# Performance work log

Measured on AMD Instinct MI355X. Metric: run time of the kernel, lower is better.

The kernel has to match this reference:

```python
import jax, jax.numpy as jnp
import numpy as np

D = 64  # hidden_dim


def _bn(x, gamma, beta):
    # eval-mode BatchNorm1d with running_mean=0, running_var=1 (fresh model)
    return gamma * x + beta


def _edge_conv(h, W, b, gamma, beta):
    # h: [B,N,D]; W: [2D,D] split into Wi (acts on x_i) and Wj (acts on x_j)
    Wi, Wj = W[:D], W[D:]
    ti = jnp.einsum('bnd,de->bne', h, Wi)  # [B,N,D] (i term)
    tj = jnp.einsum('bmd,de->bme', h, Wj)  # [B,N,D] (j term)
    # e[b,i,j,:] = x_i@Wi + x_j@Wj + b  -> relu -> BN -> max over j
    e = ti[:, :, None, :] + tj[:, None, :, :] + b  # [B,N,N,D]
    e = _bn(jax.nn.relu(e), gamma, beta)
    return e.max(axis=2)  # [B,N,D]


def setup_inputs() -> dict:
    key = jax.random.key(0)
    ks = jax.random.split(key, 16)
    s = lambda k, shp, sc: (jax.random.normal(k, shp, dtype=jnp.float32) * sc)
    inp = {
        'x': s(ks[0], (32, 256, 4), 1.0),
        'W1': s(ks[1], (4, D), 0.5), 'b1': s(ks[2], (D,), 0.1),
        'g1': 1.0 + s(ks[3], (D,), 0.1), 'beta1': s(ks[4], (D,), 0.1),
        'We1': s(ks[5], (2 * D, D), 0.1), 'be1': s(ks[6], (D,), 0.1),
        'ge1': 1.0 + s(ks[7], (D,), 0.1), 'betae1': s(ks[8], (D,), 0.1),
        'We2': s(ks[9], (2 * D, D), 0.1), 'be2': s(ks[10], (D,), 0.1),
        'ge2': 1.0 + s(ks[11], (D,), 0.1), 'betae2': s(ks[12], (D,), 0.1),
        'Wg1': s(ks[13], (2 * D, D), 0.1), 'bg1': s(ks[14], (D,), 0.1),
        'Wg2': s(ks[15], (D, 2), 0.1), 'bg2': jnp.zeros((2,), jnp.float32),
    }
    return inp


def reference(x, W1, b1, g1, beta1, We1, be1, ge1, betae1, We2, be2, ge2, betae2, Wg1, bg1, Wg2, bg2):
    # input MLP: Linear -> ReLU -> BN (eval)
    h = _bn(jax.nn.relu(x @ W1 + b1), g1, beta1)  # [B,N,D]
    h = _edge_conv(h, We1, be1, ge1, betae1)
    h = _edge_conv(h, We2, be2, ge2, betae2)
    x_mean = h.mean(axis=1)  # [B,D]
    x_max = h.max(axis=1)    # [B,D]
    xg = jnp.concatenate([x_mean, x_max], axis=-1)  # [B,2D]
    # global MLP (dropout is identity in eval)
    out = jax.nn.relu(xg @ Wg1 + bg1) @ Wg2 + bg2  # [B,2]
    return out
```

## Files before the change

### kernel.cpp

```cpp
#include <hip/hip_runtime.h>

#define NB 32
#define NN 256
#define DD 64
#define GG 4
#define NPB 64


__global__ __launch_bounds__(512) void k_conv1(
    const float* __restrict__ x,
    const float* __restrict__ W1,  const float* __restrict__ b1,
    const float* __restrict__ g1,  const float* __restrict__ beta1,
    const float* __restrict__ We1,
    float* __restrict__ TI, float* __restrict__ PMAX, float* __restrict__ PMIN)
{
    __shared__ float Hs[NPB * 65];
    const int b  = blockIdx.x >> 2;
    const int g  = blockIdx.x & 3;
    const int l  = threadIdx.x & 63;
    const int w  = __builtin_amdgcn_readfirstlane(threadIdx.x >> 6);
    const int n  = g * NPB + l;
    const int d0 = w * 8;

    {
        float4 xv = *(const float4*)(x + ((size_t)b * NN + n) * 4);
        float a[8];
#pragma unroll
        for (int j = 0; j < 8; ++j) a[j] = b1[d0 + j];
#pragma unroll
        for (int j = 0; j < 8; ++j) a[j] = fmaf(xv.x, W1[0 * DD + d0 + j], a[j]);
#pragma unroll
        for (int j = 0; j < 8; ++j) a[j] = fmaf(xv.y, W1[1 * DD + d0 + j], a[j]);
#pragma unroll
        for (int j = 0; j < 8; ++j) a[j] = fmaf(xv.z, W1[2 * DD + d0 + j], a[j]);
#pragma unroll
        for (int j = 0; j < 8; ++j) a[j] = fmaf(xv.w, W1[3 * DD + d0 + j], a[j]);
#pragma unroll
        for (int j = 0; j < 8; ++j)
            Hs[l * 65 + d0 + j] = g1[d0 + j] * fmaxf(a[j], 0.f) + beta1[d0 + j];
    }
    __syncthreads();

    float ti[8], tj[8];
#pragma unroll
    for (int j = 0; j < 8; ++j) { ti[j] = 0.f; tj[j] = 0.f; }
#pragma unroll
    for (int k = 0; k < DD; ++k) {
        const float hk = Hs[l * 65 + k];
        const float* wi = We1 + k * DD + d0;
        const float* wj = We1 + (DD + k) * DD + d0;
#pragma unroll
        for (int j = 0; j < 8; ++j) {
            ti[j] = fmaf(hk, wi[j], ti[j]);
            tj[j] = fmaf(hk, wj[j], tj[j]);
        }
    }
    {
        float* o = TI + ((size_t)(b * NN + n)) * DD + d0;
        *(float4*)(o)     = make_float4(ti[0], ti[1], ti[2], ti[3]);
        *(float4*)(o + 4) = make_float4(ti[4], ti[5], ti[6], ti[7]);
    }
    float mx[8], mn[8];
#pragma unroll
    for (int j = 0; j < 8; ++j) { mx[j] = tj[j]; mn[j] = tj[j]; }
#pragma unroll
    for (int m = 1; m < 64; m <<= 1) {
#pragma unroll
        for (int j = 0; j < 8; ++j) {
            mx[j] = fmaxf(mx[j], __shfl_xor(mx[j], m, 64));
            mn[j] = fminf(mn[j], __shfl_xor(mn[j], m, 64));
        }
    }
    float smx = mx[0], smn = mn[0];
#pragma unroll
    for (int j = 1; j < 8; ++j) {
        smx = (l == j) ? mx[j] : smx;
        smn = (l == j) ? mn[j] : smn;
    }
    if (l < 8) {
        PMAX[(b * GG + g) * DD + d0 + l] = smx;
        PMIN[(b * GG + g) * DD + d0 + l] = smn;
    }
}

__global__ __launch_bounds__(512) void k_conv2(
    const float* __restrict__ PMAXin, const float* __restrict__ PMINin,
    const float* __restrict__ beP, const float* __restrict__ geP,
    const float* __restrict__ bteP,
    const float* __restrict__ We,
    float* __restrict__ TI, float* __restrict__ PMAX, float* __restrict__ PMIN)
{
    __shared__ float Hs[NPB * 65];
    const int b  = blockIdx.x >> 2;
    const int g  = blockIdx.x & 3;
    const int l  = threadIdx.x & 63;
    const int w  = __builtin_amdgcn_readfirstlane(threadIdx.x >> 6);
    const int n  = g * NPB + l;
    const int d0 = w * 8;

    float rmax[8], rmin[8];
#pragma unroll
    for (int j = 0; j < 8; ++j) {
        rmax[j] = fmaxf(fmaxf(PMAXin[(b * GG + 0) * DD + d0 + j],
                              PMAXin[(b * GG + 1) * DD + d0 + j]),
                        fmaxf(PMAXin[(b * GG + 2) * DD + d0 + j],
                              PMAXin[(b * GG + 3) * DD + d0 + j]));
        rmin[j] = fminf(fminf(PMINin[(b * GG + 0) * DD + d0 + j],
                              PMINin[(b * GG + 1) * DD + d0 + j]),
                        fminf(PMINin[(b * GG + 2) * DD + d0 + j],
                              PMINin[(b * GG + 3) * DD + d0 + j]));
    }
    {
        const float* tip = TI + ((size_t)(b * NN + n)) * DD + d0;
        float4 t0 = *(const float4*)tip;
        float4 t1 = *(const float4*)(tip + 4);
        float tiv[8] = {t0.x, t0.y, t0.z, t0.w, t1.x, t1.y, t1.z, t1.w};
#pragma unroll
        for (int j = 0; j < 8; ++j) {
            float gv = geP[d0 + j];
            float sv = tiv[j] + (gv >= 0.f ? rmax[j] : rmin[j]) + beP[d0 + j];
            Hs[l * 65 + d0 + j] = gv * fmaxf(sv, 0.f) + bteP[d0 + j];
        }
    }
    __syncthreads();

    float ti[8], tj[8];
#pragma unroll
    for (int j = 0; j < 8; ++j) { ti[j] = 0.f; tj[j] = 0.f; }
#pragma unroll
    for (int k = 0; k < DD; ++k) {
        const float hk = Hs[l * 65 + k];
        const float* wi = We + k * DD + d0;
        const float* wj = We + (DD + k) * DD + d0;
#pragma unroll
        for (int j = 0; j < 8; ++j) {
            ti[j] = fmaf(hk, wi[j], ti[j]);
            tj[j] = fmaf(hk, wj[j], tj[j]);
        }
    }
    {
        float* o = TI + ((size_t)(b * NN + n)) * DD + d0;
        *(float4*)(o)     = make_float4(ti[0], ti[1], ti[2], ti[3]);
        *(float4*)(o + 4) = make_float4(ti[4], ti[5], ti[6], ti[7]);
    }
    float mx[8], mn[8];
#pragma unroll
    for (int j = 0; j < 8; ++j) { mx[j] = tj[j]; mn[j] = tj[j]; }
#pragma unroll
    for (int m = 1; m < 64; m <<= 1) {
#pragma unroll
        for (int j = 0; j < 8; ++j) {
            mx[j] = fmaxf(mx[j], __shfl_xor(mx[j], m, 64));
            mn[j] = fminf(mn[j], __shfl_xor(mn[j], m, 64));
        }
    }
    float smx = mx[0], smn = mn[0];
#pragma unroll
    for (int j = 1; j < 8; ++j) {
        smx = (l == j) ? mx[j] : smx;
        smn = (l == j) ? mn[j] : smn;
    }
    if (l < 8) {
        PMAX[(b * GG + g) * DD + d0 + l] = smx;
        PMIN[(b * GG + g) * DD + d0 + l] = smn;
    }
}

__global__ __launch_bounds__(512, 1) void k_poolhead(
    const float* __restrict__ PMAXin, const float* __restrict__ PMINin,
    const float* __restrict__ beP, const float* __restrict__ geP,
    const float* __restrict__ bteP,
    const float* __restrict__ TI,
    const float* __restrict__ Wg1, const float* __restrict__ bg1,
    const float* __restrict__ Wg2, const float* __restrict__ bg2,
    float* __restrict__ out)
{
    __shared__ float TT[2 * NN * 33];
    __shared__ float PA[8 * 64];
    __shared__ float PB[8 * 64];
    __shared__ float XG[2 * DD];
    __shared__ float HID[DD];

    const int b  = blockIdx.x;
    const int t  = threadIdx.x;
    const int l  = t & 63;
    const int w  = __builtin_amdgcn_readfirstlane(t >> 6);
    const int s2 = w >> 2;
    const int n  = (w & 3) * 64 + l;
    const int d0 = s2 * 32;

    float rmax[32], rmin[32];
#pragma unroll
    for (int j = 0; j < 32; ++j) {
        rmax[j] = fmaxf(fmaxf(PMAXin[(b * GG + 0) * DD + d0 + j],
                              PMAXin[(b * GG + 1) * DD + d0 + j]),
                        fmaxf(PMAXin[(b * GG + 2) * DD + d0 + j],
                              PMAXin[(b * GG + 3) * DD + d0 + j]));
        rmin[j] = fminf(fminf(PMINin[(b * GG + 0) * DD + d0 + j],
                              PMINin[(b * GG + 1) * DD + d0 + j]),
                        fminf(PMINin[(b * GG + 2) * DD + d0 + j],
                              PMINin[(b * GG + 3) * DD + d0 + j]));
    }

    {
        const float* tip = TI + ((size_t)(b * NN + n)) * DD + d0;
        float* Tw = TT + (s2 * NN + n) * 33;
#pragma unroll
        for (int j4 = 0; j4 < 8; ++j4) {
            float4 tv = ((const float4*)tip)[j4];
            float tvv[4] = {tv.x, tv.y, tv.z, tv.w};
#pragma unroll
            for (int q = 0; q < 4; ++q) {
                int j = 4 * j4 + q;
                float gv = geP[d0 + j];
                float sv = tvv[q] + (gv >= 0.f ? rmax[j] : rmin[j]) + beP[d0 + j];
                Tw[j] = gv * fmaxf(sv, 0.f) + bteP[d0 + j];
            }
        }
    }
    __syncthreads();

    {
        const int d   = t & 63;
        const int grp = t >> 6;
        const int ss  = d >> 5;
        const int jj  = d & 31;
        float sm = 0.f, mx = -3.402823466e+38f;
#pragma unroll
        for (int m = 0; m < 32; ++m) {
            float v = TT[(ss * NN + grp * 32 + m) * 33 + jj];
            sm += v;
            mx = fmaxf(mx, v);
        }
        PA[grp * 64 + d] = sm;
        PB[grp * 64 + d] = mx;
    }
    __syncthreads();
    if (t < 64) {
        float asum = PA[t], amax = PB[t];
#pragma unroll
        for (int q = 1; q < 8; ++q) {
            asum += PA[q * 64 + t];
            amax = fmaxf(amax, PB[q * 64 + t]);
        }
        XG[t]      = asum * (1.f / 256.f);
        XG[64 + t] = amax;
    }
    __syncthreads();

    if (t < 64) {
        float a = bg1[t];
#pragma unroll
        for (int k = 0; k < 2 * DD; ++k) a = fmaf(XG[k], Wg1[k * DD + t], a);
        HID[t] = fmaxf(a, 0.f);
    }
    __syncthreads();
    if (t < 2) {
        float o = bg2[t];
#pragma unroll
        for (int j = 0; j < DD; ++j) o = fmaf(HID[j], Wg2[j * 2 + t], o);
        out[b * 2 + t] = o;
    }
}

extern "C" void kernel_launch(void* const* d_in, const int* in_sizes, int n_in,
                              void* d_out, int out_size, void* d_ws, size_t ws_size,
                              hipStream_t stream) {
    const float* x     = (const float*)d_in[0];
    const float* W1    = (const float*)d_in[1];
    const float* b1    = (const float*)d_in[2];
    const float* g1    = (const float*)d_in[3];
    const float* beta1 = (const float*)d_in[4];
    const float* We1   = (const float*)d_in[5];
    const float* be1   = (const float*)d_in[6];
    const float* ge1   = (const float*)d_in[7];
    const float* bte1  = (const float*)d_in[8];
    const float* We2   = (const float*)d_in[9];
    const float* be2   = (const float*)d_in[10];
    const float* ge2   = (const float*)d_in[11];
    const float* bte2  = (const float*)d_in[12];
    const float* Wg1   = (const float*)d_in[13];
    const float* bg1   = (const float*)d_in[14];
    const float* Wg2   = (const float*)d_in[15];
    const float* bg2   = (const float*)d_in[16];

    float* ws    = (float*)d_ws;
    float* TI    = ws;
    float* PMAX1 = ws + 524288;
    float* PMIN1 = ws + 532480;
    float* PMAX2 = ws + 540672;
    float* PMIN2 = ws + 548864;

    k_conv1<<<dim3(NB * GG), dim3(512), 0, stream>>>(
        x, W1, b1, g1, beta1, We1, TI, PMAX1, PMIN1);
    k_conv2<<<dim3(NB * GG), dim3(512), 0, stream>>>(
        PMAX1, PMIN1, be1, ge1, bte1, We2, TI, PMAX2, PMIN2);
    k_poolhead<<<dim3(NB), dim3(512), 0, stream>>>(
        PMAX2, PMIN2, be2, ge2, bte2, TI, Wg1, bg1, Wg2, bg2, (float*)d_out);
}
```

Measured before the change: 123.2 us.

## Double threads per block and replace LDS transpose pooling with wave shuffles

Each block now runs 1024 threads (16 waves), and every thread in the conv kernels handles 4 output channels instead of 8. This doubles the waves available for latency hiding on a grid of only 128 blocks. The pooling kernel drops its large shared-memory transpose buffer and reduces sum and max across the 64 points in a wave with xor-shuffles, then combines the per-group partials in a small LDS array. The cost is fewer registers per thread under the 1024 bound, more shuffle instructions, and the per-thread reloads of PMAX/PMIN that are now done inline.

```diff
diff --git a/kernel.cpp b/kernel.cpp
--- a/kernel.cpp
+++ b/kernel.cpp
@@ -7,7 +7,7 @@
 #define NPB 64
 
 
-__global__ __launch_bounds__(512) void k_conv1(
+__global__ __launch_bounds__(1024) void k_conv1(
     const float* __restrict__ x,
     const float* __restrict__ W1,  const float* __restrict__ b1,
     const float* __restrict__ g1,  const float* __restrict__ beta1,
@@ -20,70 +20,66 @@
     const int l  = threadIdx.x & 63;
     const int w  = __builtin_amdgcn_readfirstlane(threadIdx.x >> 6);
     const int n  = g * NPB + l;
-    const int d0 = w * 8;
+    const int d0 = w * 4;
 
     {
         float4 xv = *(const float4*)(x + ((size_t)b * NN + n) * 4);
-        float a[8];
-#pragma unroll
-        for (int j = 0; j < 8; ++j) a[j] = b1[d0 + j];
-#pragma unroll
-        for (int j = 0; j < 8; ++j) a[j] = fmaf(xv.x, W1[0 * DD + d0 + j], a[j]);
-#pragma unroll
-        for (int j = 0; j < 8; ++j) a[j] = fmaf(xv.y, W1[1 * DD + d0 + j], a[j]);
-#pragma unroll
-        for (int j = 0; j < 8; ++j) a[j] = fmaf(xv.z, W1[2 * DD + d0 + j], a[j]);
-#pragma unroll
-        for (int j = 0; j < 8; ++j) a[j] = fmaf(xv.w, W1[3 * DD + d0 + j], a[j]);
-#pragma unroll
-        for (int j = 0; j < 8; ++j)
+        float a[4];
+#pragma unroll
+        for (int j = 0; j < 4; ++j) a[j] = b1[d0 + j];
+#pragma unroll
+        for (int j = 0; j < 4; ++j) a[j] = fmaf(xv.x, W1[0 * DD + d0 + j], a[j]);
+#pragma unroll
+        for (int j = 0; j < 4; ++j) a[j] = fmaf(xv.y, W1[1 * DD + d0 + j], a[j]);
+#pragma unroll
+        for (int j = 0; j < 4; ++j) a[j] = fmaf(xv.z, W1[2 * DD + d0 + j], a[j]);
+#pragma unroll
+        for (int j = 0; j < 4; ++j) a[j] = fmaf(xv.w, W1[3 * DD + d0 + j], a[j]);
+#pragma unroll
+        for (int j = 0; j < 4; ++j)
             Hs[l * 65 + d0 + j] = g1[d0 + j] * fmaxf(a[j], 0.f) + beta1[d0 + j];
     }
     __syncthreads();
 
-    float ti[8], tj[8];
-#pragma unroll
-    for (int j = 0; j < 8; ++j) { ti[j] = 0.f; tj[j] = 0.f; }
+    float ti[4] = {0.f, 0.f, 0.f, 0.f}, tj[4] = {0.f, 0.f, 0.f, 0.f};
 #pragma unroll
     for (int k = 0; k < DD; ++k) {
         const float hk = Hs[l * 65 + k];
         const float* wi = We1 + k * DD + d0;
         const float* wj = We1 + (DD + k) * DD + d0;
 #pragma unroll
-        for (int j = 0; j < 8; ++j) {
+        for (int j = 0; j < 4; ++j) {
             ti[j] = fmaf(hk, wi[j], ti[j]);
             tj[j] = fmaf(hk, wj[j], tj[j]);
         }
     }
-    {
-        float* o = TI + ((size_t)(b * NN + n)) * DD + d0;
-        *(float4*)(o)     = make_float4(ti[0], ti[1], ti[2], ti[3]);
-        *(float4*)(o + 4) = make_float4(ti[4], ti[5], ti[6], ti[7]);
-    }
-    float mx[8], mn[8];
-#pragma unroll
-    for (int j = 0; j < 8; ++j) { mx[j] = tj[j]; mn[j] = tj[j]; }
+    *(float4*)(TI + ((size_t)(b * NN + n)) * DD + d0) =
+        make_float4(ti[0], ti[1], ti[2], ti[3]);
+
+    float mx[4], mn[4];
+#pragma unroll
+    for (int j = 0; j < 4; ++j) { mx[j] = tj[j]; mn[j] = tj[j]; }
 #pragma unroll
     for (int m = 1; m < 64; m <<= 1) {
 #pragma unroll
-        for (int j = 0; j < 8; ++j) {
+        for (int j = 0; j < 4; ++j) {
             mx[j] = fmaxf(mx[j], __shfl_xor(mx[j], m, 64));
             mn[j] = fminf(mn[j], __shfl_xor(mn[j], m, 64));
         }
     }
     float smx = mx[0], smn = mn[0];
 #pragma unroll
-    for (int j = 1; j < 8; ++j) {
+    for (int j = 1; j < 4; ++j) {
         smx = (l == j) ? mx[j] : smx;
         smn = (l == j) ? mn[j] : smn;
     }
-    if (l < 8) {
+    if (l < 4) {
         PMAX[(b * GG + g) * DD + d0 + l] = smx;
         PMIN[(b * GG + g) * DD + d0 + l] = smn;
     }
 }
 
-__global__ __launch_bounds__(512) void k_conv2(
+__global__ __launch_bounds__(1024) void k_conv2(
     const float* __restrict__ PMAXin, const float* __restrict__ PMINin,
     const float* __restrict__ beP, const float* __restrict__ geP,
     const float* __restrict__ bteP,
@@ -96,77 +92,67 @@
     const int l  = threadIdx.x & 63;
     const int w  = __builtin_amdgcn_readfirstlane(threadIdx.x >> 6);
     const int n  = g * NPB + l;
-    const int d0 = w * 8;
-
-    float rmax[8], rmin[8];
-#pragma unroll
-    for (int j = 0; j < 8; ++j) {
-        rmax[j] = fmaxf(fmaxf(PMAXin[(b * GG + 0) * DD + d0 + j],
-                              PMAXin[(b * GG + 1) * DD + d0 + j]),
-                        fmaxf(PMAXin[(b * GG + 2) * DD + d0 + j],
-                              PMAXin[(b * GG + 3) * DD + d0 + j]));
-        rmin[j] = fminf(fminf(PMINin[(b * GG + 0) * DD + d0 + j],
-                              PMINin[(b * GG + 1) * DD + d0 + j]),
-                        fminf(PMINin[(b * GG + 2) * DD + d0 + j],
-                              PMINin[(b * GG + 3) * DD + d0 + j]));
-    }
+    const int d0 = w * 4;
+
     {
-        const float* tip = TI + ((size_t)(b * NN + n)) * DD + d0;
-        float4 t0 = *(const float4*)tip;
-        float4 t1 = *(const float4*)(tip + 4);
-        float tiv[8] = {t0.x, t0.y, t0.z, t0.w, t1.x, t1.y, t1.z, t1.w};
-#pragma unroll
-        for (int j = 0; j < 8; ++j) {
+        float4 tv = *(const float4*)(TI + ((size_t)(b * NN + n)) * DD + d0);
+        float tiv[4] = {tv.x, tv.y, tv.z, tv.w};
+#pragma unroll
+        for (int j = 0; j < 4; ++j) {
+            float rmax = fmaxf(fmaxf(PMAXin[(b * GG + 0) * DD + d0 + j],
+                                     PMAXin[(b * GG + 1) * DD + d0 + j]),
+                               fmaxf(PMAXin[(b * GG + 2) * DD + d0 + j],
+                                     PMAXin[(b * GG + 3) * DD + d0 + j]));
+            float rmin = fminf(fminf(PMINin[(b * GG + 0) * DD + d0 + j],
+                                     PMINin[(b * GG + 1) * DD + d0 + j]),
+                               fminf(PMINin[(b * GG + 2) * DD + d0 + j],
+                                     PMINin[(b * GG + 3) * DD + d0 + j]));
             float gv = geP[d0 + j];
-            float sv = tiv[j] + (gv >= 0.f ? rmax[j] : rmin[j]) + beP[d0 + j];
+            float sv = tiv[j] + (gv >= 0.f ? rmax : rmin) + beP[d0 + j];
             Hs[l * 65 + d0 + j] = gv * fmaxf(sv, 0.f) + bteP[d0 + j];
         }
     }
     __syncthreads();
 
-    float ti[8], tj[8];
-#pragma unroll
-    for (int j = 0; j < 8; ++j) { ti[j] = 0.f; tj[j] = 0.f; }
+    float ti[4] = {0.f, 0.f, 0.f, 0.f}, tj[4] = {0.f, 0.f, 0.f, 0.f};
 #pragma unroll
     for (int k = 0; k < DD; ++k) {
         const float hk = Hs[l * 65 + k];
         const float* wi = We + k * DD + d0;
         const float* wj = We + (DD + k) * DD + d0;
 #pragma unroll
-        for (int j = 0; j < 8; ++j) {
+        for (int j = 0; j < 4; ++j) {
             ti[j] = fmaf(hk, wi[j], ti[j]);
             tj[j] = fmaf(hk, wj[j], tj[j]);
         }
     }
-    {
-        float* o = TI + ((size_t)(b * NN + n)) * DD + d0;
-        *(float4*)(o)     = make_float4(ti[0], ti[1], ti[2], ti[3]);
-        *(float4*)(o + 4) = make_float4(ti[4], ti[5], ti[6], ti[7]);
-    }
-    float mx[8], mn[8];
-#pragma unroll
-    for (int j = 0; j < 8; ++j) { mx[j] = tj[j]; mn[j] = tj[j]; }
+    *(float4*)(TI + ((size_t)(b * NN + n)) * DD + d0) =
+        make_float4(ti[0], ti[1], ti[2], ti[3]);
+
+    float mx[4], mn[4];
+#pragma unroll
+    for (int j = 0; j < 4; ++j) { mx[j] = tj[j]; mn[j] = tj[j]; }
 #pragma unroll
     for (int m = 1; m < 64; m <<= 1) {
 #pragma unroll
-        for (int j = 0; j < 8; ++j) {
+        for (int j = 0; j < 4; ++j) {
             mx[j] = fmaxf(mx[j], __shfl_xor(mx[j], m, 64));
             mn[j] = fminf(mn[j], __shfl_xor(mn[j], m, 64));
         }
     }
     float smx = mx[0], smn = mn[0];
 #pragma unroll
-    for (int j = 1; j < 8; ++j) {
+    for (int j = 1; j < 4; ++j) {
         smx = (l == j) ? mx[j] : smx;
         smn = (l == j) ? mn[j] : smn;
     }
-    if (l < 8) {
+    if (l < 4) {
         PMAX[(b * GG + g) * DD + d0 + l] = smx;
         PMIN[(b * GG + g) * DD + d0 + l] = smn;
     }
 }
 
-__global__ __launch_bounds__(512, 1) void k_poolhead(
+__global__ __launch_bounds__(1024) void k_poolhead(
     const float* __restrict__ PMAXin, const float* __restrict__ PMINin,
     const float* __restrict__ beP, const float* __restrict__ geP,
     const float* __restrict__ bteP,
@@ -175,9 +161,8 @@
     const float* __restrict__ Wg2, const float* __restrict__ bg2,
     float* __restrict__ out)
 {
-    __shared__ float TT[2 * NN * 33];
-    __shared__ float PA[8 * 64];
-    __shared__ float PB[8 * 64];
+    __shared__ float PS[GG * DD];
+    __shared__ float PX[GG * DD];
     __shared__ float XG[2 * DD];
     __shared__ float HID[DD];
 
@@ -185,64 +170,60 @@
     const int t  = threadIdx.x;
     const int l  = t & 63;
     const int w  = __builtin_amdgcn_readfirstlane(t >> 6);
-    const int s2 = w >> 2;
-    const int n  = (w & 3) * 64 + l;
-    const int d0 = s2 * 32;
-
-    float rmax[32], rmin[32];
-#pragma unroll
-    for (int j = 0; j < 32; ++j) {
-        rmax[j] = fmaxf(fmaxf(PMAXin[(b * GG + 0) * DD + d0 + j],
-                              PMAXin[(b * GG + 1) * DD + d0 + j]),
-                        fmaxf(PMAXin[(b * GG + 2) * DD + d0 + j],
-                              PMAXin[(b * GG + 3) * DD + d0 + j]));
-        rmin[j] = fminf(fminf(PMINin[(b * GG + 0) * DD + d0 + j],
-                              PMINin[(b * GG + 1) * DD + d0 + j]),
-                        fminf(PMINin[(b * GG + 2) * DD + d0 + j],
-                              PMINin[(b * GG + 3) * DD + d0 + j]));
-    }
-
+    const int g3 = w & 3;
+    const int d0 = (w >> 2) * 16;
+    const int n  = g3 * 64 + l;
+
+    float sm[16], mx[16];
     {
         const float* tip = TI + ((size_t)(b * NN + n)) * DD + d0;
-        float* Tw = TT + (s2 * NN + n) * 33;
-#pragma unroll
-        for (int j4 = 0; j4 < 8; ++j4) {
+#pragma unroll
+        for (int j4 = 0; j4 < 4; ++j4) {
             float4 tv = ((const float4*)tip)[j4];
             float tvv[4] = {tv.x, tv.y, tv.z, tv.w};
 #pragma unroll
             for (int q = 0; q < 4; ++q) {
-                int j = 4 * j4 + q;
+                const int j = 4 * j4 + q;
+                float rmax = fmaxf(fmaxf(PMAXin[(b * GG + 0) * DD + d0 + j],
+                                         PMAXin[(b * GG + 1) * DD + d0 + j]),
+                                   fmaxf(PMAXin[(b * GG + 2) * DD + d0 + j],
+                                         PMAXin[(b * GG + 3) * DD + d0 + j]));
+                float rmin = fminf(fminf(PMINin[(b * GG + 0) * DD + d0 + j],
+                                         PMINin[(b * GG + 1) * DD + d0 + j]),
+                                   fminf(PMINin[(b * GG + 2) * DD + d0 + j],
+                                         PMINin[(b * GG + 3) * DD + d0 + j]));
                 float gv = geP[d0 + j];
-                float sv = tvv[q] + (gv >= 0.f ? rmax[j] : rmin[j]) + beP[d0 + j];
-                Tw[j] = gv * fmaxf(sv, 0.f) + bteP[d0 + j];
+                float sv = tvv[q] + (gv >= 0.f ? rmax : rmin) + beP[d0 + j];
+                float hv = gv * fmaxf(sv, 0.f) + bteP[d0 + j];
+                sm[j] = hv;
+                mx[j] = hv;
             }
         }
     }
-    __syncthreads();
-
-    {
-        const int d   = t & 63;
-        const int grp = t >> 6;
-        const int ss  = d >> 5;
-        const int jj  = d & 31;
-        float sm = 0.f, mx = -3.402823466e+38f;
-#pragma unroll
-        for (int m = 0; m < 32; ++m) {
-            float v = TT[(ss * NN + grp * 32 + m) * 33 + jj];
-            sm += v;
-            mx = fmaxf(mx, v);
-        }
-        PA[grp * 64 + d] = sm;
-        PB[grp * 64 + d] = mx;
-    }
-    __syncthreads();
+#pragma unroll
+    for (int m = 1; m < 64; m <<= 1) {
+#pragma unroll
+        for (int j = 0; j < 16; ++j) {
+            sm[j] += __shfl_xor(sm[j], m, 64);
+            mx[j] = fmaxf(mx[j], __shfl_xor(mx[j], m, 64));
+        }
+    }
+    float ssm = sm[0], smx = mx[0];
+#pragma unroll
+    for (int j = 1; j < 16; ++j) {
+        ssm = (l == j) ? sm[j] : ssm;
+        smx = (l == j) ? mx[j] : smx;
+    }
+    if (l < 16) {
+        PS[g3 * DD + d0 + l] = ssm;
+        PX[g3 * DD + d0 + l] = smx;
+    }
+    __syncthreads();
+
     if (t < 64) {
-        float asum = PA[t], amax = PB[t];
-#pragma unroll
-        for (int q = 1; q < 8; ++q) {
-            asum += PA[q * 64 + t];
-            amax = fmaxf(amax, PB[q * 64 + t]);
-        }
+        float asum = PS[0 * DD + t] + PS[1 * DD + t] + PS[2 * DD + t] + PS[3 * DD + t];
+        float amax = fmaxf(fmaxf(PX[0 * DD + t], PX[1 * DD + t]),
+                           fmaxf(PX[2 * DD + t], PX[3 * DD + t]));
         XG[t]      = asum * (1.f / 256.f);
         XG[64 + t] = amax;
     }
@@ -291,10 +272,10 @@
     float* PMAX2 = ws + 540672;
     float* PMIN2 = ws + 548864;
 
-    k_conv1<<<dim3(NB * GG), dim3(512), 0, stream>>>(
+    k_conv1<<<dim3(NB * GG), dim3(1024), 0, stream>>>(
         x, W1, b1, g1, beta1, We1, TI, PMAX1, PMIN1);
-    k_conv2<<<dim3(NB * GG), dim3(512), 0, stream>>>(
+    k_conv2<<<dim3(NB * GG), dim3(1024), 0, stream>>>(
         PMAX1, PMIN1, be1, ge1, bte1, We2, TI, PMAX2, PMIN2);
-    k_poolhead<<<dim3(NB), dim3(512), 0, stream>>>(
+    k_poolhead<<<dim3(NB), dim3(1024), 0, stream>>>(
         PMAX2, PMIN2, be2, ge2, bte2, TI, Wg1, bg1, Wg2, bg2, (float*)d_out);
 }
```

After: 123.9 us. About the same (+0.5%).
